# Performance work log

Hardware: AMD Instinct MI355X
Metric: run time of the kernel (lower is better)

Reference implementation:

```python
import jax, jax.numpy as jnp
import numpy as np

N_EMBD = 1024
N_HEAD = 16
MASK_FILL = -10000.0


def setup_inputs() -> dict:
    key = jax.random.key(0)
    ks = jax.random.split(key, 9)
    s = 1.0 / np.sqrt(N_EMBD)
    d = {"x": jax.random.normal(ks[0], (4, 2048, N_EMBD), dtype=jnp.float32)}
    for i, name in enumerate(["k", "q", "v", "p"]):
        d[f"W{name}"] = jax.random.uniform(ks[1 + 2 * i], (N_EMBD, N_EMBD), minval=-s, maxval=s, dtype=jnp.float32)
        d[f"b{name}"] = jax.random.uniform(ks[2 + 2 * i], (N_EMBD,), minval=-s, maxval=s, dtype=jnp.float32)
    return d


def reference(x, Wk, bk, Wq, bq, Wv, bv, Wp, bp):
    B, T, C = x.shape
    H, D = N_HEAD, C // N_HEAD
    # projections -> [B, H, T, D]
    def split_heads(y):
        return y.reshape(B, T, H, D).transpose(0, 2, 1, 3)
    k = split_heads(x @ Wk + bk)
    q = split_heads(x @ Wq + bq)
    v = split_heads(x @ Wv + bv)
    att = jnp.einsum("bhtd,bhsd->bhts", q, k) / jnp.sqrt(jnp.float32(D))
    causal = jnp.tril(jnp.ones((T, T), dtype=bool))  # [T, T]
    att = jnp.where(causal[None, None], att, MASK_FILL)
    att = jax.nn.softmax(att, axis=-1)
    y = jnp.einsum("bhts,bhsd->bhtd", att, v)
    y = y.transpose(0, 2, 1, 3).reshape(B, T, C)
    return y @ Wp + bp
```

## Files before the change

### kernel.cpp

```cpp
#include <hip/hip_runtime.h>
#include <hip/hip_bf16.h>

#define CDIM   1024
#define NHEADS 16
#define DHEAD  64
#define BATCH  4
#define TSEQ   2048
#define MROWS  (BATCH * TSEQ)
#define QSTR   3072
#define NEG_BIG (-1e30f)
#define MASKVAL (-3.0e38f)
#define SCALE_L2E 0.18033688011f
#define DEFER_TH 11.5416f

typedef __attribute__((ext_vector_type(8)))  short bf16x8;
typedef __attribute__((ext_vector_type(4)))  float f32x4;
typedef __attribute__((ext_vector_type(16))) float f32x16;

__device__ __forceinline__ unsigned short f2bf(float f) {
    __hip_bfloat16 h = __float2bfloat16(f);
    return *reinterpret_cast<unsigned short*>(&h);
}
__device__ __forceinline__ unsigned int pk2(float a, float b) {
    return (unsigned)f2bf(a) | ((unsigned)f2bf(b) << 16);
}
__device__ __forceinline__ unsigned int cvtpk(float a, float b) {
    unsigned r;
    asm("v_cvt_pk_bf16_f32 %0, %1, %2" : "=v"(r) : "v"(a), "v"(b));
    return r;
}
__device__ __forceinline__ float ex2(float x) {
    float r; asm("v_exp_f32 %0, %1" : "=v"(r) : "v"(x)); return r;
}

__global__ __launch_bounds__(256)
void cvt_x_kernel(const float* __restrict__ in, unsigned short* __restrict__ out)
{
    size_t i = (size_t)blockIdx.x * 256 + threadIdx.x;
    const float4* p = reinterpret_cast<const float4*>(in) + i * 2;
    float4 a = p[0], b = p[1];
    uint4 o;
    o.x = (unsigned)f2bf(a.x) | ((unsigned)f2bf(a.y) << 16);
    o.y = (unsigned)f2bf(a.z) | ((unsigned)f2bf(a.w) << 16);
    o.z = (unsigned)f2bf(b.x) | ((unsigned)f2bf(b.y) << 16);
    o.w = (unsigned)f2bf(b.z) | ((unsigned)f2bf(b.w) << 16);
    *reinterpret_cast<uint4*>(out + i * 8) = o;
}

__global__ __launch_bounds__(256)
void wt_kernel(const float* __restrict__ W0, const float* __restrict__ W1,
               const float* __restrict__ W2, const float* __restrict__ W3,
               unsigned short* __restrict__ T0, unsigned short* __restrict__ T1,
               unsigned short* __restrict__ T2, unsigned short* __restrict__ T3)
{
    const float* W; unsigned short* T;
    switch (blockIdx.z) {
        case 0:  W = W0; T = T0; break;
        case 1:  W = W1; T = T1; break;
        case 2:  W = W2; T = T2; break;
        default: W = W3; T = T3; break;
    }
    __shared__ float tile[32][33];
    const int t = threadIdx.x;
    const int r = t >> 3;
    const int c4 = (t & 7) * 4;
    const int n0 = blockIdx.x * 32, k0 = blockIdx.y * 32;
    float4 v = *reinterpret_cast<const float4*>(&W[(size_t)(k0 + r) * CDIM + n0 + c4]);
    tile[r][c4 + 0] = v.x; tile[r][c4 + 1] = v.y;
    tile[r][c4 + 2] = v.z; tile[r][c4 + 3] = v.w;
    __syncthreads();
    uint2 o;
    o.x = (unsigned)f2bf(tile[c4 + 0][r]) | ((unsigned)f2bf(tile[c4 + 1][r]) << 16);
    o.y = (unsigned)f2bf(tile[c4 + 2][r]) | ((unsigned)f2bf(tile[c4 + 3][r]) << 16);
    *reinterpret_cast<uint2*>(&T[(size_t)(n0 + r) * CDIM + k0 + c4]) = o;
}

__global__ __launch_bounds__(256)
void pack_bias(const float* __restrict__ bq, const float* __restrict__ bk,
               const float* __restrict__ bv, float* __restrict__ o)
{
    int i = blockIdx.x * 256 + threadIdx.x;
    float v = (i < 1024) ? bq[i] : (i < 2048 ? bk[i - 1024] : bv[i - 2048]);
    o[i] = v;
}

template<int OUTMODE>
__global__ __launch_bounds__(256)
void gemm_glds(const unsigned short* __restrict__ A,
               const unsigned short* __restrict__ BT,
               const float* __restrict__ bias,
               void* __restrict__ Cout, int M, int N, int K, int nScaled)
{
    __shared__ __align__(16) unsigned short As[128 * 32];
    __shared__ __align__(16) unsigned short Bs[128 * 32];
    const int tid = threadIdx.x;
    const int nbn = N >> 7;
    const int bid = blockIdx.x;
    const int wg  = (bid & 7) * ((int)gridDim.x >> 3) + (bid >> 3);
    const int n0  = (wg % nbn) * 128;
    const int m0  = (wg / nbn) * 128;

    const int lane = tid & 63, w = tid >> 6;
    const int wr = w >> 1, wc = w & 1;
    const int lj = lane & 15, lg = lane >> 4;
    const int rl = lane >> 2, sl = lane & 3;

    char* AsB = (char*)As;
    char* BsB = (char*)Bs;

    f32x4 acc[4][4];
    #pragma unroll
    for (int i = 0; i < 4; ++i)
        #pragma unroll
        for (int j = 0; j < 4; ++j) acc[i][j] = f32x4{0.f, 0.f, 0.f, 0.f};

    for (int k0 = 0; k0 < K; k0 += 32) {
        __syncthreads();
        #pragma unroll
        for (int t = 0; t < 2; ++t) {
            const int r = t * 64 + w * 16 + rl;
            const int g = sl ^ (r & 3);
            __builtin_amdgcn_global_load_lds(
                (const __attribute__((address_space(1))) void*)(A + (size_t)(m0 + r) * K + k0 + 8 * g),
                (__attribute__((address_space(3))) void*)(AsB + t * 4096 + w * 1024),
                16, 0, 0);
            __builtin_amdgcn_global_load_lds(
                (const __attribute__((address_space(1))) void*)(BT + (size_t)(n0 + r) * K + k0 + 8 * g),
                (__attribute__((address_space(3))) void*)(BsB + t * 4096 + w * 1024),
                16, 0, 0);
        }
        __syncthreads();
        bf16x8 af[4], bfr[4];
        #pragma unroll
        for (int i = 0; i < 4; ++i) {
            const int r = wr * 64 + i * 16 + lj;
            af[i] = *reinterpret_cast<const bf16x8*>(AsB + r * 64 + ((lg ^ (r & 3)) * 16));
        }
        #pragma unroll
        for (int j = 0; j < 4; ++j) {
            const int r = wc * 64 + j * 16 + lj;
            bfr[j] = *reinterpret_cast<const bf16x8*>(BsB + r * 64 + ((lg ^ (r & 3)) * 16));
        }
        #pragma unroll
        for (int i = 0; i < 4; ++i)
            #pragma unroll
            for (int j = 0; j < 4; ++j)
                acc[i][j] = __builtin_amdgcn_mfma_f32_16x16x32_bf16(af[i], bfr[j], acc[i][j], 0, 0, 0);
    }

    const float sc = (n0 < nScaled) ? SCALE_L2E : 1.0f;
    float bcol[4];
    #pragma unroll
    for (int j = 0; j < 4; ++j) bcol[j] = bias[n0 + wc * 64 + j * 16 + lj];

    #pragma unroll
    for (int i = 0; i < 4; ++i) {
        #pragma unroll
        for (int r4 = 0; r4 < 4; ++r4) {
            const int row = m0 + wr * 64 + i * 16 + lg * 4 + r4;
            #pragma unroll
            for (int j = 0; j < 4; ++j) {
                const int col = n0 + wc * 64 + j * 16 + lj;
                float v = (acc[i][j][r4] + bcol[j]) * sc;
                if (OUTMODE == 0)
                    reinterpret_cast<unsigned short*>(Cout)[(size_t)row * N + col] = f2bf(v);
                else
                    reinterpret_cast<float*>(Cout)[(size_t)row * N + col] = v;
            }
        }
    }
}

#define PV_STEP(m, T, rb) { \
    unsigned int w01 = cvtpk(T[(rb)+0], T[(rb)+1]); \
    unsigned int w23 = cvtpk(T[(rb)+2], T[(rb)+3]); \
    unsigned int w45 = cvtpk(T[(rb)+4], T[(rb)+5]); \
    unsigned int w67 = cvtpk(T[(rb)+6], T[(rb)+7]); \
    asm("v_permlane32_swap_b32 %0, %1" : "+v"(w01), "+v"(w45)); \
    asm("v_permlane32_swap_b32 %0, %1" : "+v"(w23), "+v"(w67)); \
    union { unsigned int u[4]; bf16x8 v; } pa; \
    pa.u[0] = w01; pa.u[1] = w23; pa.u[2] = w45; pa.u[3] = w67; \
    const int voff = (32 * (m) + 16 * hi) ^ lqswz; \
    bf16x8 va = *reinterpret_cast<const bf16x8*>(VTB + lq * 128 + voff); \
    bf16x8 vb = *reinterpret_cast<const bf16x8*>(VTB + (lq + 32) * 128 + voff); \
    y0 = __builtin_amdgcn_mfma_f32_32x32x16_bf16(va, pa.v, y0, 0, 0, 0); \
    y1 = __builtin_amdgcn_mfma_f32_32x32x16_bf16(vb, pa.v, y1, 0, 0, 0); \
}

__global__ __launch_bounds__(256)
void attn_mfma6(const unsigned short* __restrict__ QKV, unsigned short* __restrict__ Yb)
{
    __shared__ unsigned short Ks[64 * 64];
    __shared__ unsigned short VTs[64 * 64];
    __shared__ unsigned short Ysc[4][32 * 72];

    const int tid = threadIdx.x, lane = tid & 63, wid = tid >> 6;
    const int lq = lane & 31, hi = lane >> 5;
    const int lqswz = (lq & 7) << 4;

    const int id  = blockIdx.x;
    const int kk  = id >> 3;
    const int hb  = (id & 7) + 8 * (kk >> 3);
    const int pair = kk & 7;
    const int h = hb & 15, bz = hb >> 4;

    const size_t rowbase = (size_t)bz * TSEQ;
    const int hq = h * DHEAD, hk = 1024 + h * DHEAD, hv = 2048 + h * DHEAD;
    char* KsB = (char*)Ks;
    char* VTB = (char*)VTs;

    const int krow = tid >> 3;
    const int kswz = ((tid & 7) * 16) ^ ((krow & 7) << 4);
    const int vk2  = 2 * (tid & 31);
    const int vdg  = (tid >> 5) * 8;
    const int vkb  = vk2 * 2;

    for (int iter = 0; iter < 2; ++iter) {
        const int qtile = iter ? (15 - pair) : pair;
        const int q0 = qtile * 128;
        const int wq = q0 + wid * 32;

        bf16x8 qf[4];
        {
            const unsigned short* qp = QKV + (rowbase + wq + lq) * QSTR + hq + hi * 8;
            #pragma unroll
            for (int s = 0; s < 4; ++s)
                qf[s] = *reinterpret_cast<const bf16x8*>(qp + s * 16);
        }
        f32x16 y0, y1;
        #pragma unroll
        for (int r = 0; r < 16; ++r) { y0[r] = 0.f; y1[r] = 0.f; }
        float mrow = NEG_BIG, lrow = 0.f;

        const int ktend = 2 * qtile + 2;

        uint4 kr0, kr1, vr0, vr1;
        {
            const unsigned short* kp = QKV + (rowbase + krow) * QSTR + hk + (tid & 7) * 8;
            kr0 = *reinterpret_cast<const uint4*>(kp);
            kr1 = *reinterpret_cast<const uint4*>(kp + 32 * QSTR);
            const unsigned short* vp = QKV + (rowbase + vk2) * QSTR + hv + vdg;
            vr0 = *reinterpret_cast<const uint4*>(vp);
            vr1 = *reinterpret_cast<const uint4*>(vp + QSTR);
        }

        for (int kt = 0; kt < ktend; ++kt) {
            __syncthreads();
            *reinterpret_cast<uint4*>(KsB + krow * 128 + kswz) = kr0;
            *reinterpret_cast<uint4*>(KsB + (krow + 32) * 128 + kswz) = kr1;
            {
                unsigned pe, po;
                pe = __builtin_amdgcn_perm(vr1.x, vr0.x, 0x05040100u);
                po = __builtin_amdgcn_perm(vr1.x, vr0.x, 0x07060302u);
                *reinterpret_cast<unsigned*>(VTB + (vdg + 0) * 128 + (vkb ^ 0x00)) = pe;
                *reinterpret_cast<unsigned*>(VTB + (vdg + 1) * 128 + (vkb ^ 0x10)) = po;
                pe = __builtin_amdgcn_perm(vr1.y, vr0.y, 0x05040100u);
                po = __builtin_amdgcn_perm(vr1.y, vr0.y, 0x07060302u);
                *reinterpret_cast<unsigned*>(VTB + (vdg + 2) * 128 + (vkb ^ 0x20)) = pe;
                *reinterpret_cast<unsigned*>(VTB + (vdg + 3) * 128 + (vkb ^ 0x30)) = po;
                pe = __builtin_amdgcn_perm(vr1.z, vr0.z, 0x05040100u);
                po = __builtin_amdgcn_perm(vr1.z, vr0.z, 0x07060302u);
                *reinterpret_cast<unsigned*>(VTB + (vdg + 4) * 128 + (vkb ^ 0x40)) = pe;
                *reinterpret_cast<unsigned*>(VTB + (vdg + 5) * 128 + (vkb ^ 0x50)) = po;
                pe = __builtin_amdgcn_perm(vr1.w, vr0.w, 0x05040100u);
                po = __builtin_amdgcn_perm(vr1.w, vr0.w, 0x07060302u);
                *reinterpret_cast<unsigned*>(VTB + (vdg + 6) * 128 + (vkb ^ 0x60)) = pe;
                *reinterpret_cast<unsigned*>(VTB + (vdg + 7) * 128 + (vkb ^ 0x70)) = po;
            }
            __syncthreads();

            if (kt + 1 < ktend) {
                const unsigned short* kp = QKV + (rowbase + (kt + 1) * 64 + krow) * QSTR + hk + (tid & 7) * 8;
                kr0 = *reinterpret_cast<const uint4*>(kp);
                kr1 = *reinterpret_cast<const uint4*>(kp + 32 * QSTR);
                const unsigned short* vp = QKV + (rowbase + (kt + 1) * 64 + vk2) * QSTR + hv + vdg;
                vr0 = *reinterpret_cast<const uint4*>(vp);
                vr1 = *reinterpret_cast<const uint4*>(vp + QSTR);
            }

            if (kt * 64 > wq + 31) continue;

            f32x16 s0, s1;
            #pragma unroll
            for (int r = 0; r < 16; ++r) { s0[r] = 0.f; s1[r] = 0.f; }
            #pragma unroll
            for (int s = 0; s < 4; ++s) {
                const int off = (s * 32 + hi * 16) ^ lqswz;
                bf16x8 k0 = *reinterpret_cast<const bf16x8*>(KsB + lq * 128 + off);
                bf16x8 k1 = *reinterpret_cast<const bf16x8*>(KsB + (lq + 32) * 128 + off);
                s0 = __builtin_amdgcn_mfma_f32_32x32x16_bf16(k0, qf[s], s0, 0, 0, 0);
                s1 = __builtin_amdgcn_mfma_f32_32x32x16_bf16(k1, qf[s], s1, 0, 0, 0);
            }

            const bool diag = (kt * 64 + 63) > wq;
            if (diag) {
                const int q_own = wq + lq;
                #pragma unroll
                for (int r = 0; r < 16; ++r) {
                    const int kl = kt * 64 + (r & 3) + 8 * (r >> 2) + 4 * hi;
                    if (kl > q_own) s0[r] = MASKVAL;
                    if (kl + 32 > q_own) s1[r] = MASKVAL;
                }
            }

            float t8[8];
            #pragma unroll
            for (int r = 0; r < 8; ++r)
                t8[r] = fmaxf(fmaxf(s0[r], s0[r + 8]), fmaxf(s1[r], s1[r + 8]));
            #pragma unroll
            for (int r = 0; r < 4; ++r) t8[r] = fmaxf(t8[r], t8[r + 4]);
            float pm = fmaxf(fmaxf(t8[0], t8[1]), fmaxf(t8[2], t8[3]));
            pm = fmaxf(pm, __shfl_xor(pm, 32));

            if (__any(pm > mrow + DEFER_TH)) {
                const float mnew = fmaxf(mrow, pm);
                const float alpha = ex2(mrow - mnew);
                #pragma unroll
                for (int r = 0; r < 16; ++r) { y0[r] *= alpha; y1[r] *= alpha; }
                lrow *= alpha;
                mrow = mnew;
            }
            #pragma unroll
            for (int r = 0; r < 16; ++r) {
                s0[r] = ex2(s0[r] - mrow);
                s1[r] = ex2(s1[r] - mrow);
            }
            float a8[8];
            #pragma unroll
            for (int r = 0; r < 8; ++r) a8[r] = (s0[r] + s0[r + 8]) + (s1[r] + s1[r + 8]);
            #pragma unroll
            for (int r = 0; r < 4; ++r) a8[r] += a8[r + 4];
            float sum = (a8[0] + a8[1]) + (a8[2] + a8[3]);
            sum += __shfl_xor(sum, 32);
            lrow += sum;

            PV_STEP(0, s0, 0)
            PV_STEP(1, s0, 8)
            PV_STEP(2, s1, 0)
            PV_STEP(3, s1, 8)
        }

        {
            const float inv = 1.f / lrow;
            char* ysb = (char*)&Ysc[wid][0];
            #pragma unroll
            for (int t = 0; t < 8; ++t) {
                const int dl = ((2 * t) & 3) + 8 * (t >> 1) + 4 * hi;
                unsigned int wa = cvtpk(y0[2 * t] * inv, y0[2 * t + 1] * inv);
                unsigned int wb = cvtpk(y1[2 * t] * inv, y1[2 * t + 1] * inv);
                *reinterpret_cast<unsigned int*>(ysb + lq * 144 + dl * 2) = wa;
                *reinterpret_cast<unsigned int*>(ysb + lq * 144 + (dl + 32) * 2) = wb;
            }
            #pragma unroll
            for (int u = 0; u < 4; ++u) {
                const int rr = lane >> 1, ch = (lane & 1) + 2 * u;
                uint4 val = *reinterpret_cast<const uint4*>(ysb + rr * 144 + ch * 16);
                *reinterpret_cast<uint4*>(Yb + (rowbase + q0 + wid * 32 + rr) * CDIM + h * DHEAD + ch * 8) = val;
            }
        }
    }
}

extern "C" void kernel_launch(void* const* d_in, const int* in_sizes, int n_in,
                              void* d_out, int out_size, void* d_ws, size_t ws_size,
                              hipStream_t stream)
{
    const float* x  = (const float*)d_in[0];
    const float* Wk = (const float*)d_in[1];
    const float* bk = (const float*)d_in[2];
    const float* Wq = (const float*)d_in[3];
    const float* bq = (const float*)d_in[4];
    const float* Wv = (const float*)d_in[5];
    const float* bv = (const float*)d_in[6];
    const float* Wp = (const float*)d_in[7];
    const float* bp = (const float*)d_in[8];

    const size_t xe = (size_t)MROWS * CDIM;
    const size_t we = (size_t)CDIM * CDIM;
    unsigned short* xb    = (unsigned short*)d_ws;
    unsigned short* wqkvt = xb + xe;
    unsigned short* wpt   = wqkvt + 3 * we;
    unsigned short* qkv   = wpt + we;
    unsigned short* ab    = qkv + (size_t)MROWS * QSTR;
    float*          bias3 = (float*)(ab + xe);

    cvt_x_kernel<<<(int)(xe / 8 / 256), 256, 0, stream>>>(x, xb);
    wt_kernel<<<dim3(32, 32, 4), 256, 0, stream>>>(
        Wq, Wk, Wv, Wp, wqkvt, wqkvt + we, wqkvt + 2 * we, wpt);
    pack_bias<<<12, 256, 0, stream>>>(bq, bk, bv, bias3);

    gemm_glds<0><<<24 * 64, 256, 0, stream>>>(xb, wqkvt, bias3, qkv,
                                              MROWS, QSTR, CDIM, 1024);

    attn_mfma6<<<512, 256, 0, stream>>>(qkv, ab);

    gemm_glds<1><<<8 * 64, 256, 0, stream>>>(ab, wpt, bp, d_out,
                                             MROWS, CDIM, CDIM, 0);
}
```

Before: 183.7 us.

## Split attention KV range across two wave groups and double GEMM K-step

The attention kernel now launches 512 threads per block as two groups of four waves. Each group processes alternate 64-key tiles in its own LDS buffers, and the two partial softmax states (max, sum, output accumulators) are merged through LDS at the end. This doubles the parallelism per query tile and shortens the serial KV loop, at the cost of an extra merge step and more LDS and register pressure. Separately, the GEMM K-tile grows from 32 to 64 with a new 8-way XOR swizzle, halving the number of barrier iterations per output tile.

```diff
diff --git a/kernel.cpp b/kernel.cpp
--- a/kernel.cpp
+++ b/kernel.cpp
@@ -20,9 +20,6 @@
 __device__ __forceinline__ unsigned short f2bf(float f) {
     __hip_bfloat16 h = __float2bfloat16(f);
     return *reinterpret_cast<unsigned short*>(&h);
-}
-__device__ __forceinline__ unsigned int pk2(float a, float b) {
-    return (unsigned)f2bf(a) | ((unsigned)f2bf(b) << 16);
 }
 __device__ __forceinline__ unsigned int cvtpk(float a, float b) {
     unsigned r;
@@ -91,8 +88,8 @@
                const float* __restrict__ bias,
                void* __restrict__ Cout, int M, int N, int K, int nScaled)
 {
-    __shared__ __align__(16) unsigned short As[128 * 32];
-    __shared__ __align__(16) unsigned short Bs[128 * 32];
+    __shared__ __align__(16) unsigned short As[128 * 64];
+    __shared__ __align__(16) unsigned short Bs[128 * 64];
     const int tid = threadIdx.x;
     const int nbn = N >> 7;
     const int bid = blockIdx.x;
@@ -103,7 +100,8 @@
     const int lane = tid & 63, w = tid >> 6;
     const int wr = w >> 1, wc = w & 1;
     const int lj = lane & 15, lg = lane >> 4;
-    const int rl = lane >> 2, sl = lane & 3;
+    const int srow = w * 8 + (lane >> 3);
+    const int gsw  = 8 * ((lane & 7) ^ (lane >> 3));
 
     char* AsB = (char*)As;
     char* BsB = (char*)Bs;
@@ -114,38 +112,42 @@
         #pragma unroll
         for (int j = 0; j < 4; ++j) acc[i][j] = f32x4{0.f, 0.f, 0.f, 0.f};
 
-    for (int k0 = 0; k0 < K; k0 += 32) {
+    for (int k0 = 0; k0 < K; k0 += 64) {
         __syncthreads();
         #pragma unroll
-        for (int t = 0; t < 2; ++t) {
-            const int r = t * 64 + w * 16 + rl;
-            const int g = sl ^ (r & 3);
+        for (int ra = 0; ra < 4; ++ra) {
+            const int r = ra * 32 + srow;
             __builtin_amdgcn_global_load_lds(
-                (const __attribute__((address_space(1))) void*)(A + (size_t)(m0 + r) * K + k0 + 8 * g),
-                (__attribute__((address_space(3))) void*)(AsB + t * 4096 + w * 1024),
+                (const __attribute__((address_space(1))) void*)(A + (size_t)(m0 + r) * K + k0 + gsw),
+                (__attribute__((address_space(3))) void*)(AsB + ra * 4096 + w * 1024),
                 16, 0, 0);
             __builtin_amdgcn_global_load_lds(
-                (const __attribute__((address_space(1))) void*)(BT + (size_t)(n0 + r) * K + k0 + 8 * g),
-                (__attribute__((address_space(3))) void*)(BsB + t * 4096 + w * 1024),
+                (const __attribute__((address_space(1))) void*)(BT + (size_t)(n0 + r) * K + k0 + gsw),
+                (__attribute__((address_space(3))) void*)(BsB + ra * 4096 + w * 1024),
                 16, 0, 0);
         }
         __syncthreads();
-        bf16x8 af[4], bfr[4];
         #pragma unroll
-        for (int i = 0; i < 4; ++i) {
-            const int r = wr * 64 + i * 16 + lj;
-            af[i] = *reinterpret_cast<const bf16x8*>(AsB + r * 64 + ((lg ^ (r & 3)) * 16));
-        }
-        #pragma unroll
-        for (int j = 0; j < 4; ++j) {
-            const int r = wc * 64 + j * 16 + lj;
-            bfr[j] = *reinterpret_cast<const bf16x8*>(BsB + r * 64 + ((lg ^ (r & 3)) * 16));
-        }
-        #pragma unroll
-        for (int i = 0; i < 4; ++i)
-            #pragma unroll
-            for (int j = 0; j < 4; ++j)
-                acc[i][j] = __builtin_amdgcn_mfma_f32_16x16x32_bf16(af[i], bfr[j], acc[i][j], 0, 0, 0);
+        for (int ks = 0; ks < 2; ++ks) {
+            bf16x8 af[4], bfr[4];
+            #pragma unroll
+            for (int i = 0; i < 4; ++i) {
+                const int r = wr * 64 + i * 16 + lj;
+                af[i] = *reinterpret_cast<const bf16x8*>(
+                    AsB + r * 128 + (((ks * 4 + lg) ^ (lj & 7)) * 16));
+            }
+            #pragma unroll
+            for (int j = 0; j < 4; ++j) {
+                const int r = wc * 64 + j * 16 + lj;
+                bfr[j] = *reinterpret_cast<const bf16x8*>(
+                    BsB + r * 128 + (((ks * 4 + lg) ^ (lj & 7)) * 16));
+            }
+            #pragma unroll
+            for (int i = 0; i < 4; ++i)
+                #pragma unroll
+                for (int j = 0; j < 4; ++j)
+                    acc[i][j] = __builtin_amdgcn_mfma_f32_16x16x32_bf16(af[i], bfr[j], acc[i][j], 0, 0, 0);
+        }
     }
 
     const float sc = (n0 < nScaled) ? SCALE_L2E : 1.0f;
@@ -187,16 +189,17 @@
     y1 = __builtin_amdgcn_mfma_f32_32x32x16_bf16(vb, pa.v, y1, 0, 0, 0); \
 }
 
-__global__ __launch_bounds__(256)
-void attn_mfma6(const unsigned short* __restrict__ QKV, unsigned short* __restrict__ Yb)
-{
-    __shared__ unsigned short Ks[64 * 64];
-    __shared__ unsigned short VTs[64 * 64];
+__global__ __launch_bounds__(512, 4)
+void attn_mfma7(const unsigned short* __restrict__ QKV, unsigned short* __restrict__ Yb)
+{
+    __shared__ __align__(16) char ldsG[2][16384];
     __shared__ unsigned short Ysc[4][32 * 72];
 
     const int tid = threadIdx.x, lane = tid & 63, wid = tid >> 6;
+    const int grp = wid >> 2, cw = wid & 3;
     const int lq = lane & 31, hi = lane >> 5;
     const int lqswz = (lq & 7) << 4;
+    const int tg = tid & 255;
 
     const int id  = blockIdx.x;
     const int kk  = id >> 3;
@@ -206,19 +209,20 @@
 
     const size_t rowbase = (size_t)bz * TSEQ;
     const int hq = h * DHEAD, hk = 1024 + h * DHEAD, hv = 2048 + h * DHEAD;
-    char* KsB = (char*)Ks;
-    char* VTB = (char*)VTs;
-
-    const int krow = tid >> 3;
-    const int kswz = ((tid & 7) * 16) ^ ((krow & 7) << 4);
-    const int vk2  = 2 * (tid & 31);
-    const int vdg  = (tid >> 5) * 8;
+    char* KsB = &ldsG[grp][0];
+    char* VTB = &ldsG[grp][8192];
+
+    const int krow = tg >> 3;
+    const int kcol8 = (tg & 7) * 8;
+    const int kswz = ((tg & 7) * 16) ^ ((krow & 7) << 4);
+    const int vk2  = 2 * (tg & 31);
+    const int vdg  = (tg >> 5) * 8;
     const int vkb  = vk2 * 2;
 
     for (int iter = 0; iter < 2; ++iter) {
         const int qtile = iter ? (15 - pair) : pair;
         const int q0 = qtile * 128;
-        const int wq = q0 + wid * 32;
+        const int wq = q0 + cw * 32;
 
         bf16x8 qf[4];
         {
@@ -232,19 +236,20 @@
         for (int r = 0; r < 16; ++r) { y0[r] = 0.f; y1[r] = 0.f; }
         float mrow = NEG_BIG, lrow = 0.f;
 
-        const int ktend = 2 * qtile + 2;
+        const int nIt = qtile + 1;
 
         uint4 kr0, kr1, vr0, vr1;
         {
-            const unsigned short* kp = QKV + (rowbase + krow) * QSTR + hk + (tid & 7) * 8;
+            const unsigned short* kp = QKV + (rowbase + grp * 64 + krow) * QSTR + hk + kcol8;
             kr0 = *reinterpret_cast<const uint4*>(kp);
             kr1 = *reinterpret_cast<const uint4*>(kp + 32 * QSTR);
-            const unsigned short* vp = QKV + (rowbase + vk2) * QSTR + hv + vdg;
+            const unsigned short* vp = QKV + (rowbase + grp * 64 + vk2) * QSTR + hv + vdg;
             vr0 = *reinterpret_cast<const uint4*>(vp);
             vr1 = *reinterpret_cast<const uint4*>(vp + QSTR);
         }
 
-        for (int kt = 0; kt < ktend; ++kt) {
+        for (int i = 0; i < nIt; ++i) {
+            const int ktg = 2 * i + grp;
             __syncthreads();
             *reinterpret_cast<uint4*>(KsB + krow * 128 + kswz) = kr0;
             *reinterpret_cast<uint4*>(KsB + (krow + 32) * 128 + kswz) = kr1;
@@ -269,16 +274,17 @@
             }
             __syncthreads();
 
-            if (kt + 1 < ktend) {
-                const unsigned short* kp = QKV + (rowbase + (kt + 1) * 64 + krow) * QSTR + hk + (tid & 7) * 8;
+            if (i + 1 < nIt) {
+                const int ktn = 2 * (i + 1) + grp;
+                const unsigned short* kp = QKV + (rowbase + ktn * 64 + krow) * QSTR + hk + kcol8;
                 kr0 = *reinterpret_cast<const uint4*>(kp);
                 kr1 = *reinterpret_cast<const uint4*>(kp + 32 * QSTR);
-                const unsigned short* vp = QKV + (rowbase + (kt + 1) * 64 + vk2) * QSTR + hv + vdg;
+                const unsigned short* vp = QKV + (rowbase + ktn * 64 + vk2) * QSTR + hv + vdg;
                 vr0 = *reinterpret_cast<const uint4*>(vp);
                 vr1 = *reinterpret_cast<const uint4*>(vp + QSTR);
             }
 
-            if (kt * 64 > wq + 31) continue;
+            if (ktg * 64 > wq + 31) continue;
 
             f32x16 s0, s1;
             #pragma unroll
@@ -292,12 +298,12 @@
                 s1 = __builtin_amdgcn_mfma_f32_32x32x16_bf16(k1, qf[s], s1, 0, 0, 0);
             }
 
-            const bool diag = (kt * 64 + 63) > wq;
+            const bool diag = (ktg * 64 + 63) > wq;
             if (diag) {
                 const int q_own = wq + lq;
                 #pragma unroll
                 for (int r = 0; r < 16; ++r) {
-                    const int kl = kt * 64 + (r & 3) + 8 * (r >> 2) + 4 * hi;
+                    const int kl = ktg * 64 + (r & 3) + 8 * (r >> 2) + 4 * hi;
                     if (kl > q_own) s0[r] = MASKVAL;
                     if (kl + 32 > q_own) s1[r] = MASKVAL;
                 }
@@ -340,9 +346,34 @@
             PV_STEP(3, s1, 8)
         }
 
-        {
+        __syncthreads();
+        if (grp == 1) {
+            char* mb = (char*)ldsG + cw * 8192;
+            #pragma unroll
+            for (int r = 0; r < 16; ++r) {
+                *reinterpret_cast<float*>(mb + r * 256 + lane * 4) = y0[r];
+                *reinterpret_cast<float*>(mb + 4096 + r * 256 + lane * 4) = y1[r];
+            }
+            float2* ml = reinterpret_cast<float2*>(&Ysc[cw][0]);
+            ml[lane] = float2{mrow, lrow};
+        }
+        __syncthreads();
+        if (grp == 0) {
+            char* mb = (char*)ldsG + cw * 8192;
+            const float2 ml = reinterpret_cast<const float2*>(&Ysc[cw][0])[lane];
+            const float mN = fmaxf(mrow, ml.x);
+            const float a0 = ex2(mrow - mN), a1 = ex2(ml.x - mN);
+            lrow = lrow * a0 + ml.y * a1;
+            mrow = mN;
+            #pragma unroll
+            for (int r = 0; r < 16; ++r) {
+                float z0 = *reinterpret_cast<const float*>(mb + r * 256 + lane * 4);
+                float z1 = *reinterpret_cast<const float*>(mb + 4096 + r * 256 + lane * 4);
+                y0[r] = y0[r] * a0 + z0 * a1;
+                y1[r] = y1[r] * a0 + z1 * a1;
+            }
             const float inv = 1.f / lrow;
-            char* ysb = (char*)&Ysc[wid][0];
+            char* ysb = (char*)&Ysc[cw][0];
             #pragma unroll
             for (int t = 0; t < 8; ++t) {
                 const int dl = ((2 * t) & 3) + 8 * (t >> 1) + 4 * hi;
@@ -355,7 +386,7 @@
             for (int u = 0; u < 4; ++u) {
                 const int rr = lane >> 1, ch = (lane & 1) + 2 * u;
                 uint4 val = *reinterpret_cast<const uint4*>(ysb + rr * 144 + ch * 16);
-                *reinterpret_cast<uint4*>(Yb + (rowbase + q0 + wid * 32 + rr) * CDIM + h * DHEAD + ch * 8) = val;
+                *reinterpret_cast<uint4*>(Yb + (rowbase + q0 + cw * 32 + rr) * CDIM + h * DHEAD + ch * 8) = val;
             }
         }
     }
@@ -392,7 +423,7 @@
     gemm_glds<0><<<24 * 64, 256, 0, stream>>>(xb, wqkvt, bias3, qkv,
                                               MROWS, QSTR, CDIM, 1024);
 
-    attn_mfma6<<<512, 256, 0, stream>>>(qkv, ab);
+    attn_mfma7<<<512, 512, 0, stream>>>(qkv, ab);
 
     gemm_glds<1><<<8 * 64, 256, 0, stream>>>(ab, wpt, bp, d_out,
                                              MROWS, CDIM, CDIM, 0);
```

Result: slower. 196.3 us (+6.8%).

## Replace projection GEMMs with double-buffered 512-thread 256x128 tile kernel

Applied to the files above, without the earlier changes.

Replaces the single-buffered 128x128 GEMM with a 512-thread kernel that uses 128x256 or 256x128 tiles, BK=64 and a double-buffered LDS ping-pong. Global-to-LDS staging for the next K chunk is interleaved with the MFMA phases, and s_setprio is raised around the MFMAs. The aim is to hide load latency behind compute and raise data reuse per tile. K is hardcoded to 1024 (16 steps) and the barriers are hand-placed, which reduces generality and needs careful synchronisation.

```diff
diff --git a/kernel.cpp b/kernel.cpp
--- a/kernel.cpp
+++ b/kernel.cpp
@@ -20,9 +20,6 @@
 __device__ __forceinline__ unsigned short f2bf(float f) {
     __hip_bfloat16 h = __float2bfloat16(f);
     return *reinterpret_cast<unsigned short*>(&h);
-}
-__device__ __forceinline__ unsigned int pk2(float a, float b) {
-    return (unsigned)f2bf(a) | ((unsigned)f2bf(b) << 16);
 }
 __device__ __forceinline__ unsigned int cvtpk(float a, float b) {
     unsigned r;
@@ -84,29 +81,86 @@
     o[i] = v;
 }
 
-template<int OUTMODE>
-__global__ __launch_bounds__(256)
-void gemm_glds(const unsigned short* __restrict__ A,
+
+#define GBAR8  asm volatile("s_barrier" ::: "memory")
+#define LGKM0  asm volatile("s_waitcnt lgkmcnt(0)" ::: "memory")
+#define VMC0   asm volatile("s_waitcnt vmcnt(0)" ::: "memory")
+
+#define STAGE8(bufp, off, srcp) do { \
+    __builtin_amdgcn_global_load_lds( \
+        (const __attribute__((address_space(1))) void*)(srcp), \
+        (__attribute__((address_space(3))) void*)((bufp) + (off) + wv * 1024), 16, 0, 0); \
+    __builtin_amdgcn_global_load_lds( \
+        (const __attribute__((address_space(1))) void*)((srcp) + 65536), \
+        (__attribute__((address_space(3))) void*)((bufp) + (off) + 8192 + wv * 1024), 16, 0, 0); \
+} while (0)
+
+#define LDA_ALL(Ab) do { \
+    _Pragma("unroll") for (int m_ = 0; m_ < 4; ++m_) { \
+        const int rl_ = wr * 64 + m_ * 16 + lj; \
+        _Pragma("unroll") for (int k_ = 0; k_ < 2; ++k_) \
+            af[m_][k_] = *reinterpret_cast<const bf16x8*>( \
+                (Ab) + rl_ * 128 + (((k_ * 4 + lg) ^ (lj & 7)) * 16)); \
+    } } while (0)
+
+#define LDB_PAIR(Bb, pairi) do { \
+    _Pragma("unroll") for (int n_ = 0; n_ < 2; ++n_) { \
+        const int rl_ = wc * 64 + ((pairi) * 2 + n_) * 16 + lj; \
+        _Pragma("unroll") for (int k_ = 0; k_ < 2; ++k_) \
+            bfr[n_][k_] = *reinterpret_cast<const bf16x8*>( \
+                (Bb) + rl_ * 128 + (((k_ * 4 + lg) ^ (lj & 7)) * 16)); \
+    } } while (0)
+
+#define MM_PAIR(npair) do { \
+    __builtin_amdgcn_s_setprio(1); \
+    _Pragma("unroll") for (int m_ = 0; m_ < 4; ++m_) \
+        _Pragma("unroll") for (int n_ = 0; n_ < 2; ++n_) \
+            _Pragma("unroll") for (int k_ = 0; k_ < 2; ++k_) \
+                acc[m_][(npair) * 2 + n_] = \
+                    __builtin_amdgcn_mfma_f32_16x16x32_bf16( \
+                        af[m_][k_], bfr[n_][k_], acc[m_][(npair) * 2 + n_], 0, 0, 0); \
+    __builtin_amdgcn_s_setprio(0); \
+} while (0)
+
+template<int BM, int BN, int OUTMODE>
+__global__ __launch_bounds__(512)
+void gemm_8ph2(const unsigned short* __restrict__ A,
                const unsigned short* __restrict__ BT,
                const float* __restrict__ bias,
-               void* __restrict__ Cout, int M, int N, int K, int nScaled)
-{
-    __shared__ __align__(16) unsigned short As[128 * 32];
-    __shared__ __align__(16) unsigned short Bs[128 * 32];
+               void* __restrict__ Cout, int N, int nScaled)
+{
+    constexpr int WN = BN / 64;
+    constexpr bool A_SMALL = (BM == 128);
+    constexpr int AOFF = 0;
+    constexpr int BOFF = BM * 128;
+    constexpr int SOFF   = A_SMALL ? AOFF : BOFF;
+    constexpr int LLOOFF = A_SMALL ? BOFF : AOFF;
+    constexpr int LHIOFF = LLOOFF + 16384;
+
+    __shared__ __align__(16) char lds8[2][(BM + BN) * 128];
     const int tid = threadIdx.x;
-    const int nbn = N >> 7;
+    const int nbn = N / BN;
     const int bid = blockIdx.x;
     const int wg  = (bid & 7) * ((int)gridDim.x >> 3) + (bid >> 3);
-    const int n0  = (wg % nbn) * 128;
-    const int m0  = (wg / nbn) * 128;
-
-    const int lane = tid & 63, w = tid >> 6;
-    const int wr = w >> 1, wc = w & 1;
+    const int n0  = (wg % nbn) * BN;
+    const int m0  = (wg / nbn) * BM;
+
+    const int lane = tid & 63, wv = tid >> 6;
+    const int wr = wv / WN, wc = wv % WN;
     const int lj = lane & 15, lg = lane >> 4;
-    const int rl = lane >> 2, sl = lane & 3;
-
-    char* AsB = (char*)As;
-    char* BsB = (char*)Bs;
+    const int srow = tid >> 3;
+    const int gsw  = 8 * ((tid & 7) ^ ((tid >> 3) & 7));
+
+    char* buf0 = &lds8[0][0];
+    char* buf1 = &lds8[1][0];
+
+    const unsigned short* Sm  = A_SMALL ? A : BT;
+    const int             sb  = A_SMALL ? m0 : n0;
+    const unsigned short* Lm  = A_SMALL ? BT : A;
+    const int             lb  = A_SMALL ? n0 : m0;
+    const unsigned short* Ss  = Sm + (size_t)(sb + srow) * 1024 + gsw;
+    const unsigned short* Llo = Lm + (size_t)(lb + srow) * 1024 + gsw;
+    const unsigned short* Lhi = Lm + (size_t)(lb + 128 + srow) * 1024 + gsw;
 
     f32x4 acc[4][4];
     #pragma unroll
@@ -114,54 +168,59 @@
         #pragma unroll
         for (int j = 0; j < 4; ++j) acc[i][j] = f32x4{0.f, 0.f, 0.f, 0.f};
 
-    for (int k0 = 0; k0 < K; k0 += 32) {
-        __syncthreads();
-        #pragma unroll
-        for (int t = 0; t < 2; ++t) {
-            const int r = t * 64 + w * 16 + rl;
-            const int g = sl ^ (r & 3);
-            __builtin_amdgcn_global_load_lds(
-                (const __attribute__((address_space(1))) void*)(A + (size_t)(m0 + r) * K + k0 + 8 * g),
-                (__attribute__((address_space(3))) void*)(AsB + t * 4096 + w * 1024),
-                16, 0, 0);
-            __builtin_amdgcn_global_load_lds(
-                (const __attribute__((address_space(1))) void*)(BT + (size_t)(n0 + r) * K + k0 + 8 * g),
-                (__attribute__((address_space(3))) void*)(BsB + t * 4096 + w * 1024),
-                16, 0, 0);
-        }
-        __syncthreads();
-        bf16x8 af[4], bfr[4];
-        #pragma unroll
-        for (int i = 0; i < 4; ++i) {
-            const int r = wr * 64 + i * 16 + lj;
-            af[i] = *reinterpret_cast<const bf16x8*>(AsB + r * 64 + ((lg ^ (r & 3)) * 16));
-        }
-        #pragma unroll
-        for (int j = 0; j < 4; ++j) {
-            const int r = wc * 64 + j * 16 + lj;
-            bfr[j] = *reinterpret_cast<const bf16x8*>(BsB + r * 64 + ((lg ^ (r & 3)) * 16));
-        }
-        #pragma unroll
-        for (int i = 0; i < 4; ++i)
-            #pragma unroll
-            for (int j = 0; j < 4; ++j)
-                acc[i][j] = __builtin_amdgcn_mfma_f32_16x16x32_bf16(af[i], bfr[j], acc[i][j], 0, 0, 0);
+    STAGE8(buf0, SOFF,   Ss);
+    STAGE8(buf0, LLOOFF, Llo);
+    STAGE8(buf0, LHIOFF, Lhi);
+    VMC0; GBAR8;
+
+    bf16x8 af[4][2], bfr[2][2];
+
+    for (int it = 0; it < 8; ++it) {
+        const int e = 2 * it, o = e + 1;
+        const bool se = (e + 2) < 16;
+
+        {
+            char* Ab = buf0 + AOFF;
+            char* Bb = buf0 + BOFF;
+            LDA_ALL(Ab); LDB_PAIR(Bb, 0);
+            STAGE8(buf1, SOFF,   Ss  + o * 64);
+            STAGE8(buf1, LLOOFF, Llo + o * 64);
+            GBAR8; LGKM0; MM_PAIR(0); GBAR8;
+            LDB_PAIR(Bb, 1);
+            STAGE8(buf1, LHIOFF, Lhi + o * 64);
+            GBAR8; LGKM0; MM_PAIR(1);
+            VMC0; GBAR8;
+        }
+        {
+            char* Ab = buf1 + AOFF;
+            char* Bb = buf1 + BOFF;
+            LDA_ALL(Ab); LDB_PAIR(Bb, 0);
+            if (se) STAGE8(buf0, SOFF, Ss + (e + 2) * 64);
+            GBAR8; LGKM0; MM_PAIR(0); GBAR8;
+            LDB_PAIR(Bb, 1);
+            if (se) {
+                STAGE8(buf0, LLOOFF, Llo + (e + 2) * 64);
+                STAGE8(buf0, LHIOFF, Lhi + (e + 2) * 64);
+            }
+            GBAR8; LGKM0; MM_PAIR(1);
+            VMC0; GBAR8;
+        }
     }
 
-    const float sc = (n0 < nScaled) ? SCALE_L2E : 1.0f;
+    const float sc = (OUTMODE == 0 && n0 < nScaled) ? SCALE_L2E : 1.0f;
     float bcol[4];
     #pragma unroll
-    for (int j = 0; j < 4; ++j) bcol[j] = bias[n0 + wc * 64 + j * 16 + lj];
+    for (int nr = 0; nr < 4; ++nr) bcol[nr] = bias[n0 + wc * 64 + nr * 16 + lj];
 
     #pragma unroll
-    for (int i = 0; i < 4; ++i) {
+    for (int mr = 0; mr < 4; ++mr) {
         #pragma unroll
         for (int r4 = 0; r4 < 4; ++r4) {
-            const int row = m0 + wr * 64 + i * 16 + lg * 4 + r4;
-            #pragma unroll
-            for (int j = 0; j < 4; ++j) {
-                const int col = n0 + wc * 64 + j * 16 + lj;
-                float v = (acc[i][j][r4] + bcol[j]) * sc;
+            const int row = m0 + wr * 64 + mr * 16 + lg * 4 + r4;
+            #pragma unroll
+            for (int nr = 0; nr < 4; ++nr) {
+                const int col = n0 + wc * 64 + nr * 16 + lj;
+                float v = (acc[mr][nr][r4] + bcol[nr]) * sc;
                 if (OUTMODE == 0)
                     reinterpret_cast<unsigned short*>(Cout)[(size_t)row * N + col] = f2bf(v);
                 else
@@ -389,11 +448,11 @@
         Wq, Wk, Wv, Wp, wqkvt, wqkvt + we, wqkvt + 2 * we, wpt);
     pack_bias<<<12, 256, 0, stream>>>(bq, bk, bv, bias3);
 
-    gemm_glds<0><<<24 * 64, 256, 0, stream>>>(xb, wqkvt, bias3, qkv,
-                                              MROWS, QSTR, CDIM, 1024);
+    gemm_8ph2<128, 256, 0><<<768, 512, 0, stream>>>(xb, wqkvt, bias3, qkv,
+                                                    QSTR, 1024);
 
     attn_mfma6<<<512, 256, 0, stream>>>(qkv, ab);
 
-    gemm_glds<1><<<8 * 64, 256, 0, stream>>>(ab, wpt, bp, d_out,
-                                             MROWS, CDIM, CDIM, 0);
-}
+    gemm_8ph2<256, 128, 1><<<256, 512, 0, stream>>>(ab, wpt, bp, d_out,
+                                                    CDIM, 0);
+}
```

Result: faster. 169.1 us (-7.9%).
